# Performance work log

Hardware: AMD Instinct MI355X
Metric: run time of the kernel (lower is better)

Reference implementation:

```python
import jax, jax.numpy as jnp
import numpy as np

N = 100000
E = 1600000
IN_C, HID_C, OUT_C = 128, 256, 40


def sage_conv(x, src, dst, W_l, W_r, b):
    # mean aggregation of source-node features into destination nodes
    msgs = x[src]                                            # [E, d]
    agg = jax.ops.segment_sum(msgs, dst, num_segments=N)     # [N, d]
    deg = jax.ops.segment_sum(jnp.ones((src.shape[0],), x.dtype), dst,
                              num_segments=N)                # [N]
    agg = agg / jnp.clip(deg, 1.0, None)[:, None]
    # out = lin_l(agg) + lin_r(x); weights stored [out, in] like torch
    return agg @ W_l.T + x @ W_r.T + b


def setup_inputs() -> dict:
    key = jax.random.key(0)
    ks = jax.random.split(key, 10)
    s = 0.05
    x = jax.random.normal(ks[0], (N, IN_C), dtype=jnp.float32)
    edge_index = jax.random.randint(ks[1], (2, E), 0, N, dtype=jnp.int64)
    return {
        "x": x,
        "edge_index": edge_index,
        "W_l0": jax.random.normal(ks[2], (HID_C, IN_C), dtype=jnp.float32) * s,
        "W_r0": jax.random.normal(ks[3], (HID_C, IN_C), dtype=jnp.float32) * s,
        "b0": jnp.zeros((HID_C,), jnp.float32),
        "W_l1": jax.random.normal(ks[4], (HID_C, HID_C), dtype=jnp.float32) * s,
        "W_r1": jax.random.normal(ks[5], (HID_C, HID_C), dtype=jnp.float32) * s,
        "b1": jnp.zeros((HID_C,), jnp.float32),
        "W_lo": jax.random.normal(ks[6], (OUT_C, HID_C), dtype=jnp.float32) * s,
        "W_ro": jax.random.normal(ks[7], (OUT_C, HID_C), dtype=jnp.float32) * s,
        "bo": jnp.zeros((OUT_C,), jnp.float32),
    }


def reference(x, edge_index, W_l0, W_r0, b0, W_l1, W_r1, b1, W_lo, W_ro, bo):
    src, dst = edge_index[0], edge_index[1]
    h = jax.nn.relu(sage_conv(x, src, dst, W_l0, W_r0, b0))
    h = jax.nn.relu(sage_conv(h, src, dst, W_l1, W_r1, b1))
    out = sage_conv(h, src, dst, W_lo, W_ro, bo)
    return jax.nn.log_softmax(out, axis=1)
```

## Files before the change

### kernel.cpp

```cpp
#include <hip/hip_runtime.h>
#include <hip/hip_bf16.h>
#include <cstdint>
#include <cstddef>

#define NN   100000
#define NE   1600000
#define HID  256
#define OUTC 40

typedef __attribute__((ext_vector_type(8))) short bf16x8;
typedef __attribute__((ext_vector_type(4))) float f32x4;

static __device__ __forceinline__ ushort f2bf(float f) {
    __hip_bfloat16 h = __float2bfloat16(f);
    return *reinterpret_cast<ushort*>(&h);
}
static __device__ __forceinline__ float bflo(unsigned u) { return __uint_as_float(u << 16); }
static __device__ __forceinline__ float bfhi(unsigned u) { return __uint_as_float(u & 0xffff0000u); }
static __device__ __forceinline__ float sb(unsigned w, int k) {
    return (float)((int)(w << (24 - 8 * k)) >> 24);
}

__global__ void k_count(const int* __restrict__ dst, int* __restrict__ cnt) {
    int i = blockIdx.x * blockDim.x + threadIdx.x;
    if (i < NE) atomicAdd(&cnt[dst[i]], 1);
}

__global__ void k_blocksum(const int* __restrict__ cnt, int* __restrict__ bsum) {
    __shared__ int s[256];
    int t = threadIdx.x;
    int n = blockIdx.x * 256 + t;
    s[t] = (n < NN) ? cnt[n] : 0;
    __syncthreads();
    for (int off = 128; off; off >>= 1) {
        if (t < off) s[t] += s[t + off];
        __syncthreads();
    }
    if (t == 0) bsum[blockIdx.x] = s[0];
}

__global__ void k_scanblock(const int* __restrict__ bsum, int* __restrict__ boff, int nb) {
    __shared__ int s[512];
    int t = threadIdx.x;
    int v = (t < nb) ? bsum[t] : 0;
    s[t] = v;
    __syncthreads();
    for (int off = 1; off < 512; off <<= 1) {
        int u = (t >= off) ? s[t - off] : 0;
        __syncthreads();
        s[t] += u;
        __syncthreads();
    }
    if (t < nb) boff[t] = s[t] - v;
}

__global__ void k_rowptr(const int* __restrict__ cnt, const int* __restrict__ boff,
                         int* __restrict__ rowptr, int* __restrict__ fillp,
                         float* __restrict__ invd) {
    __shared__ int s[256];
    int t = threadIdx.x;
    int n = blockIdx.x * 256 + t;
    int c = (n < NN) ? cnt[n] : 0;
    s[t] = c;
    __syncthreads();
    for (int off = 1; off < 256; off <<= 1) {
        int u = (t >= off) ? s[t - off] : 0;
        __syncthreads();
        s[t] += u;
        __syncthreads();
    }
    if (n < NN) {
        int excl = boff[blockIdx.x] + s[t] - c;
        rowptr[n] = excl;
        fillp[n]  = excl;
        invd[n]   = 1.0f / (float)(c > 1 ? c : 1);
    }
    if (n == 0) rowptr[NN] = NE;
}

__global__ void k_fill(const int* __restrict__ src, const int* __restrict__ dst,
                       int* __restrict__ fillp, int* __restrict__ colidx) {
    int i = blockIdx.x * blockDim.x + threadIdx.x;
    if (i < NE) {
        int p = atomicAdd(&fillp[dst[i]], 1);
        colidx[p] = src[i];
    }
}

__global__ void k_cvtfrag(const float* __restrict__ W, ushort* __restrict__ dst,
                          int ocreal, int d, int nf) {
    int f = blockIdx.x * 256 + threadIdx.x;
    if (f >= nf) return;
    int lm = f & 15, lk = (f >> 4) & 3;
    int rest = f >> 6;
    int dk = d / 32;
    int kk = rest % dk, cc = rest / dk;
    int row = cc * 16 + lm, col = kk * 32 + lk * 8;
    unsigned q0 = 0, q1 = 0, q2 = 0, q3 = 0;
    if (row < ocreal) {
        const float4* p = (const float4*)(W + (size_t)row * d + col);
        float4 a = p[0], b = p[1];
        q0 = (unsigned)f2bf(a.x) | ((unsigned)f2bf(a.y) << 16);
        q1 = (unsigned)f2bf(a.z) | ((unsigned)f2bf(a.w) << 16);
        q2 = (unsigned)f2bf(b.x) | ((unsigned)f2bf(b.y) << 16);
        q3 = (unsigned)f2bf(b.z) | ((unsigned)f2bf(b.w) << 16);
    }
    *(uint4*)(dst + (size_t)f * 8) = make_uint4(q0, q1, q2, q3);
}

__global__ __launch_bounds__(256) void k_quant_x4(const float* __restrict__ x,
                                                  unsigned* __restrict__ xq4,
                                                  float* __restrict__ sx4) {
    int t = threadIdx.x;
    int qw = t >> 4, ql = t & 15;
    int row = blockIdx.x * 16 + qw;
    if (row >= NN) return;
    const float4* p = (const float4*)(x + (size_t)row * 128 + ql * 8);
    float4 a = p[0], b = p[1];
    float v[8] = {a.x, a.y, a.z, a.w, b.x, b.y, b.z, b.w};
    float m = 0.f;
    #pragma unroll
    for (int k = 0; k < 8; ++k) m = fmaxf(m, fabsf(v[k]));
    m = fmaxf(m, __shfl_xor(m, 1));
    m = fmaxf(m, __shfl_xor(m, 2));
    m = fmaxf(m, __shfl_xor(m, 4));
    m = fmaxf(m, __shfl_xor(m, 8));
    float inv = (m > 0.f) ? 7.f / m : 0.f;
    unsigned w = 0;
    #pragma unroll
    for (int k = 0; k < 8; ++k)
        w |= ((unsigned)(int)rintf(v[k] * inv) & 15u) << (4 * k);
    xq4[(size_t)row * 16 + ql] = w;
    if (ql == 0) sx4[row] = (m > 0.f) ? m / 7.f : 0.f;
}

__global__ __launch_bounds__(256) void k_quant_h84(const ushort* __restrict__ h,
                                                   char* __restrict__ hq8, float* __restrict__ s8,
                                                   unsigned* __restrict__ hq4, float* __restrict__ s4) {
    int t = threadIdx.x;
    int qw = t >> 4, ql = t & 15;
    int row = blockIdx.x * 16 + qw;
    if (row >= NN) return;
    const uint4* p = (const uint4*)(h + (size_t)row * 256 + ql * 16);
    uint4 a = p[0], b = p[1];
    float v[16];
    v[0]  = bflo(a.x); v[1]  = bfhi(a.x); v[2]  = bflo(a.y); v[3]  = bfhi(a.y);
    v[4]  = bflo(a.z); v[5]  = bfhi(a.z); v[6]  = bflo(a.w); v[7]  = bfhi(a.w);
    v[8]  = bflo(b.x); v[9]  = bfhi(b.x); v[10] = bflo(b.y); v[11] = bfhi(b.y);
    v[12] = bflo(b.z); v[13] = bfhi(b.z); v[14] = bflo(b.w); v[15] = bfhi(b.w);
    float m = 0.f;
    #pragma unroll
    for (int k = 0; k < 16; ++k) m = fmaxf(m, v[k]);
    m = fmaxf(m, __shfl_xor(m, 1));
    m = fmaxf(m, __shfl_xor(m, 2));
    m = fmaxf(m, __shfl_xor(m, 4));
    m = fmaxf(m, __shfl_xor(m, 8));
    float inv8 = (m > 0.f) ? 127.f / m : 0.f;
    float inv4 = (m > 0.f) ? 15.f / m : 0.f;
    unsigned wo[4];
    #pragma unroll
    for (int wi = 0; wi < 4; ++wi) {
        unsigned w = 0;
        #pragma unroll
        for (int k = 0; k < 4; ++k)
            w |= ((unsigned)(unsigned char)(char)(int)rintf(v[wi * 4 + k] * inv8)) << (8 * k);
        wo[wi] = w;
    }
    *(uint4*)(hq8 + (size_t)row * 256 + ql * 16) = make_uint4(wo[0], wo[1], wo[2], wo[3]);
    unsigned lo = 0, hi = 0;
    #pragma unroll
    for (int k = 0; k < 8; ++k)
        lo |= ((unsigned)(int)rintf(v[k] * inv4) & 15u) << (4 * k);
    #pragma unroll
    for (int k = 0; k < 8; ++k)
        hi |= ((unsigned)(int)rintf(v[8 + k] * inv4) & 15u) << (4 * k);
    *(uint2*)(hq4 + (size_t)row * 32 + ql * 2) = make_uint2(lo, hi);
    if (ql == 0) {
        s8[row] = (m > 0.f) ? m / 127.f : 0.f;
        s4[row] = (m > 0.f) ? m / 15.f  : 0.f;
    }
}

template<int D, bool SELF_F32, bool SIGNED>
__global__ __launch_bounds__(256, 4) void k_layer4(
    const unsigned* __restrict__ qin4, const float* __restrict__ qs4,
    const void* __restrict__ selfp, const float* __restrict__ selfs,
    const ushort* __restrict__ Wl, const ushort* __restrict__ Wr,
    const float* __restrict__ bias, const float* __restrict__ invd,
    const int* __restrict__ rowptr, const int* __restrict__ colidx,
    ushort* __restrict__ hout)
{
    __shared__ ushort aggS[64 * D];
    __shared__ int cidxS[2048];
    char* aggSb = (char*)aggS;
    const int t  = threadIdx.x;
    const int r0 = blockIdx.x * 64;
    constexpr int LPR = D / 16;
    constexpr int GPB = 256 / LPR;
    constexpr int RW  = D / 8;
    const int gid = t / LPR, li = t % LPR;

    const int ebase = rowptr[r0];
    const int rend  = (r0 + 64 < NN) ? (r0 + 64) : NN;
    const int etot  = rowptr[rend] - ebase;
    const bool inlds = (etot <= 2048);
    if (inlds) {
        for (int i = t; i < etot; i += 256) cidxS[i] = colidx[ebase + i];
    }
    __syncthreads();

    for (int rr = gid; rr < 64; rr += GPB) {
        const int r = r0 + rr;
        float acc[16];
        #pragma unroll
        for (int k = 0; k < 16; ++k) acc[k] = 0.f;
        if (r < NN) {
            const int beg = rowptr[r], end = rowptr[r + 1];
            for (int e = beg; e < end; e += 8) {
                int sidx[8];
                if (inlds) {
                    #pragma unroll
                    for (int j = 0; j < 8; ++j)
                        sidx[j] = (e + j < end) ? cidxS[e + j - ebase] : -1;
                } else {
                    #pragma unroll
                    for (int j = 0; j < 8; ++j)
                        sidx[j] = (e + j < end) ? colidx[e + j] : -1;
                }
                uint2 u[8]; float sc[8];
                #pragma unroll
                for (int j = 0; j < 8; ++j) {
                    if (sidx[j] >= 0) {
                        u[j]  = *(const uint2*)(qin4 + (size_t)sidx[j] * RW + li * 2);
                        sc[j] = qs4[sidx[j]];
                    } else { u[j] = make_uint2(0u, 0u); sc[j] = 0.f; }
                }
                #pragma unroll
                for (int j = 0; j < 8; ++j) {
                    #pragma unroll
                    for (int wi = 0; wi < 2; ++wi) {
                        unsigned w = wi ? u[j].y : u[j].x;
                        #pragma unroll
                        for (int k = 0; k < 8; ++k) {
                            float f;
                            if (SIGNED) f = (float)((int)(w << (28 - 4 * k)) >> 28);
                            else        f = (float)((w >> (4 * k)) & 15u);
                            acc[wi * 8 + k] = fmaf(sc[j], f, acc[wi * 8 + k]);
                        }
                    }
                }
            }
            const float iv = invd[r];
            #pragma unroll
            for (int k = 0; k < 16; ++k) acc[k] *= iv;
        }
        #pragma unroll
        for (int gg = 0; gg < 2; ++gg) {
            unsigned q0 = (unsigned)f2bf(acc[gg*8+0]) | ((unsigned)f2bf(acc[gg*8+1]) << 16);
            unsigned q1 = (unsigned)f2bf(acc[gg*8+2]) | ((unsigned)f2bf(acc[gg*8+3]) << 16);
            unsigned q2 = (unsigned)f2bf(acc[gg*8+4]) | ((unsigned)f2bf(acc[gg*8+5]) << 16);
            unsigned q3 = (unsigned)f2bf(acc[gg*8+6]) | ((unsigned)f2bf(acc[gg*8+7]) << 16);
            int g  = li * 2 + gg;
            int gs = g ^ (rr & 7);
            *(uint4*)(aggSb + (size_t)rr * (D * 2) + (gs << 4)) = make_uint4(q0, q1, q2, q3);
        }
    }
    __syncthreads();

    const int w = t >> 6, l = t & 63, lm = l & 15, lk = l >> 4;
    const int rr = w * 16 + lm;
    const int rg = r0 + rr;

    bf16x8 ax[D / 32];
    if (SELF_F32) {
        const float* xf = (const float*)selfp;
        #pragma unroll
        for (int kk = 0; kk < D / 32; ++kk) {
            bf16x8 v;
            if (rg < NN) {
                const float4* p = (const float4*)(xf + (size_t)rg * D + kk * 32 + lk * 8);
                float4 f0 = p[0], f1 = p[1];
                v[0] = (short)f2bf(f0.x); v[1] = (short)f2bf(f0.y);
                v[2] = (short)f2bf(f0.z); v[3] = (short)f2bf(f0.w);
                v[4] = (short)f2bf(f1.x); v[5] = (short)f2bf(f1.y);
                v[6] = (short)f2bf(f1.z); v[7] = (short)f2bf(f1.w);
            } else v = (bf16x8)(short)0;
            ax[kk] = v;
        }
    } else {
        const char* hq = (const char*)selfp;
        const float sr = (rg < NN) ? selfs[rg] : 0.f;
        #pragma unroll
        for (int kk = 0; kk < D / 32; ++kk) {
            uint2 uq = (rg < NN)
                ? *(const uint2*)(hq + (size_t)rg * D + kk * 32 + lk * 8)
                : make_uint2(0u, 0u);
            bf16x8 v;
            v[0] = (short)f2bf(sr * sb(uq.x, 0));
            v[1] = (short)f2bf(sr * sb(uq.x, 1));
            v[2] = (short)f2bf(sr * sb(uq.x, 2));
            v[3] = (short)f2bf(sr * sb(uq.x, 3));
            v[4] = (short)f2bf(sr * sb(uq.y, 0));
            v[5] = (short)f2bf(sr * sb(uq.y, 1));
            v[6] = (short)f2bf(sr * sb(uq.y, 2));
            v[7] = (short)f2bf(sr * sb(uq.y, 3));
            ax[kk] = v;
        }
    }

    for (int cc = 0; cc < HID / 16; ++cc) {
        const int c = cc * 16 + lm;
        f32x4 acc = {0.f, 0.f, 0.f, 0.f};
        #pragma unroll
        for (int kk = 0; kk < D / 32; ++kk) {
            int g  = kk * 4 + lk;
            int gs = g ^ (rr & 7);
            bf16x8 a_agg = *(const bf16x8*)(aggSb + (size_t)rr * (D * 2) + (gs << 4));
            const size_t wf = ((size_t)(cc * (D / 32) + kk) * 64 + l) * 8;
            bf16x8 bl = *(const bf16x8*)(Wl + wf);
            bf16x8 br = *(const bf16x8*)(Wr + wf);
            acc = __builtin_amdgcn_mfma_f32_16x16x32_bf16(a_agg, bl, acc, 0, 0, 0);
            acc = __builtin_amdgcn_mfma_f32_16x16x32_bf16(ax[kk], br, acc, 0, 0, 0);
        }
        const float bv = bias[c];
        #pragma unroll
        for (int i = 0; i < 4; ++i) {
            const int orow = r0 + w * 16 + lk * 4 + i;
            if (orow < NN) {
                float v = fmaxf(acc[i] + bv, 0.f);
                hout[(size_t)orow * HID + c] = f2bf(v);
            }
        }
    }
}

__global__ __launch_bounds__(256, 4) void k_premul(
    const ushort* __restrict__ h1, const ushort* __restrict__ wlo,
    const ushort* __restrict__ wro, const float* __restrict__ bo,
    char* __restrict__ qq, float* __restrict__ sq, float* __restrict__ rbuf)
{
    const int t = threadIdx.x;
    const int r0 = blockIdx.x * 64;
    const int w = t >> 6, l = t & 63, lm = l & 15, lk = l >> 4;
    const int rr = w * 16 + lm;
    const int rg = r0 + rr;

    f32x4 aq[3], ar[3];
    #pragma unroll
    for (int cc = 0; cc < 3; ++cc) { aq[cc] = {0.f,0.f,0.f,0.f}; ar[cc] = {0.f,0.f,0.f,0.f}; }

    #pragma unroll
    for (int kk = 0; kk < 8; ++kk) {
        bf16x8 a = (rg < NN)
            ? *(const bf16x8*)(h1 + (size_t)rg * 256 + kk * 32 + lk * 8)
            : (bf16x8)(short)0;
        #pragma unroll
        for (int cc = 0; cc < 3; ++cc) {
            const size_t wf = ((size_t)(cc * 8 + kk) * 64 + l) * 8;
            bf16x8 bl = *(const bf16x8*)(wlo + wf);
            bf16x8 br = *(const bf16x8*)(wro + wf);
            aq[cc] = __builtin_amdgcn_mfma_f32_16x16x32_bf16(a, bl, aq[cc], 0, 0, 0);
            ar[cc] = __builtin_amdgcn_mfma_f32_16x16x32_bf16(a, br, ar[cc], 0, 0, 0);
        }
    }

    #pragma unroll
    for (int i = 0; i < 4; ++i) {
        const int orow = r0 + w * 16 + lk * 4 + i;
        if (orow >= NN) continue;
        float m = 0.f;
        #pragma unroll
        for (int cc = 0; cc < 3; ++cc) {
            const int c = cc * 16 + lm;
            if (c < OUTC) m = fmaxf(m, fabsf(aq[cc][i]));
        }
        m = fmaxf(m, __shfl_xor(m, 1));
        m = fmaxf(m, __shfl_xor(m, 2));
        m = fmaxf(m, __shfl_xor(m, 4));
        m = fmaxf(m, __shfl_xor(m, 8));
        const float inv = (m > 0.f) ? 127.f / m : 0.f;
        #pragma unroll
        for (int cc = 0; cc < 3; ++cc) {
            const int c = cc * 16 + lm;
            char qv = (c < OUTC) ? (char)(int)rintf(aq[cc][i] * inv) : (char)0;
            qq[(size_t)orow * 64 + c] = qv;
            rbuf[(size_t)orow * 64 + c] = (c < OUTC) ? (ar[cc][i] + bo[c]) : 0.f;
        }
        qq[(size_t)orow * 64 + 48 + lm] = (char)0;
        rbuf[(size_t)orow * 64 + 48 + lm] = 0.f;
        if (lm == 0) sq[orow] = m / 127.f;
    }
}

__global__ __launch_bounds__(256) void k_final(
    const char* __restrict__ qq, const float* __restrict__ sq,
    const float* __restrict__ rbuf, const float* __restrict__ invd,
    const int* __restrict__ rowptr, const int* __restrict__ colidx,
    float* __restrict__ out)
{
    const int t = threadIdx.x;
    const int g = t >> 2, li = t & 3;
    const int row = blockIdx.x * 64 + g;
    if (row >= NN) return;

    float acc[16];
    #pragma unroll
    for (int k = 0; k < 16; ++k) acc[k] = 0.f;

    const int beg = rowptr[row], end = rowptr[row + 1];
    for (int e = beg; e < end; e += 8) {
        int sidx[8];
        #pragma unroll
        for (int j = 0; j < 8; ++j) sidx[j] = (e + j < end) ? colidx[e + j] : -1;
        uint4 u[8]; float sc[8];
        #pragma unroll
        for (int j = 0; j < 8; ++j) {
            if (sidx[j] >= 0) {
                u[j]  = *(const uint4*)(qq + (size_t)sidx[j] * 64 + li * 16);
                sc[j] = sq[sidx[j]];
            } else { u[j] = make_uint4(0u, 0u, 0u, 0u); sc[j] = 0.f; }
        }
        #pragma unroll
        for (int j = 0; j < 8; ++j) {
            #pragma unroll
            for (int wi = 0; wi < 4; ++wi) {
                unsigned w = (&u[j].x)[wi];
                acc[wi*4+0] = fmaf(sc[j], sb(w, 0), acc[wi*4+0]);
                acc[wi*4+1] = fmaf(sc[j], sb(w, 1), acc[wi*4+1]);
                acc[wi*4+2] = fmaf(sc[j], sb(w, 2), acc[wi*4+2]);
                acc[wi*4+3] = fmaf(sc[j], sb(w, 3), acc[wi*4+3]);
            }
        }
    }

    const float iv = invd[row];
    const float4* rp = (const float4*)(rbuf + (size_t)row * 64 + li * 16);
    float v[16];
    #pragma unroll
    for (int ch = 0; ch < 4; ++ch) {
        float4 rv = rp[ch];
        v[ch*4+0] = acc[ch*4+0] * iv + rv.x;
        v[ch*4+1] = acc[ch*4+1] * iv + rv.y;
        v[ch*4+2] = acc[ch*4+2] * iv + rv.z;
        v[ch*4+3] = acc[ch*4+3] * iv + rv.w;
    }
    #pragma unroll
    for (int k = 0; k < 16; ++k)
        if (li * 16 + k >= OUTC) v[k] = -INFINITY;

    float m = v[0];
    #pragma unroll
    for (int k = 1; k < 16; ++k) m = fmaxf(m, v[k]);
    m = fmaxf(m, __shfl_xor(m, 1));
    m = fmaxf(m, __shfl_xor(m, 2));

    float s = 0.f;
    #pragma unroll
    for (int k = 0; k < 16; ++k)
        if (li * 16 + k < OUTC) s += __expf(v[k] - m);
    s += __shfl_xor(s, 1);
    s += __shfl_xor(s, 2);
    const float ls = __logf(s);

    #pragma unroll
    for (int ch = 0; ch < 4; ++ch) {
        const int c = li * 16 + ch * 4;
        if (c < OUTC) {
            float4 o;
            o.x = v[ch*4+0] - m - ls;
            o.y = v[ch*4+1] - m - ls;
            o.z = v[ch*4+2] - m - ls;
            o.w = v[ch*4+3] - m - ls;
            *(float4*)(out + (size_t)row * OUTC + c) = o;
        }
    }
}

extern "C" void kernel_launch(void* const* d_in, const int* in_sizes, int n_in,
                              void* d_out, int out_size, void* d_ws, size_t ws_size,
                              hipStream_t stream) {
    const float* x   = (const float*)d_in[0];
    const int*   ei  = (const int*)d_in[1];
    const int*   src = ei;
    const int*   dst = ei + NE;
    const float* Wl0 = (const float*)d_in[2];
    const float* Wr0 = (const float*)d_in[3];
    const float* b0  = (const float*)d_in[4];
    const float* Wl1 = (const float*)d_in[5];
    const float* Wr1 = (const float*)d_in[6];
    const float* b1  = (const float*)d_in[7];
    const float* Wlo = (const float*)d_in[8];
    const float* Wro = (const float*)d_in[9];
    const float* bo  = (const float*)d_in[10];
    float* out = (float*)d_out;

    char* ws = (char*)d_ws;
    const size_t MB = 1 << 20;
    float*    invd   = (float*)(ws + 0);
    int*      rowptr = (int*)(ws + MB / 2);
    int*      cnt    = (int*)(ws + MB);
    int*      fillp  = (int*)(ws + MB + MB / 2);
    int*      bsum   = (int*)(ws + 2 * MB);
    int*      boff   = (int*)(ws + 2 * MB + MB / 4);
    float*    sx4    = (float*)(ws + 2 * MB + MB / 2);
    float*    s8     = (float*)(ws + 3 * MB);
    float*    s4     = (float*)(ws + 3 * MB + MB / 2);
    float*    sq     = (float*)(ws + 4 * MB);
    ushort*   Wb     = (ushort*)(ws + 4 * MB + MB / 2);
    int*      colidx = (int*)(ws + 5 * MB + MB / 2);
    unsigned* xq4    = (unsigned*)(ws + 12 * MB);
    char*     qq     = (char*)(ws + 12 * MB);
    unsigned* h0q4   = (unsigned*)(ws + 19 * MB);
    ushort*   h0     = (ushort*)(ws + 32 * MB);
    ushort*   h1     = (ushort*)(ws + 32 * MB);
    char*     h0q8   = (char*)(ws + 84 * MB);
    float*    rbuf   = (float*)(ws + 84 * MB);

    ushort* wl0 = Wb;
    ushort* wr0 = Wb + 32768;
    ushort* wl1 = Wb + 65536;
    ushort* wr1 = Wb + 131072;
    ushort* wlo = Wb + 196608;
    ushort* wro = Wb + 208896;

    hipMemsetAsync(cnt, 0, NN * sizeof(int), stream);
    k_count<<<(NE + 255) / 256, 256, 0, stream>>>(dst, cnt);
    const int NB = (NN + 255) / 256;
    k_blocksum<<<NB, 256, 0, stream>>>(cnt, bsum);
    k_scanblock<<<1, 512, 0, stream>>>(bsum, boff, NB);
    k_rowptr<<<NB, 256, 0, stream>>>(cnt, boff, rowptr, fillp, invd);
    k_fill<<<(NE + 255) / 256, 256, 0, stream>>>(src, dst, fillp, colidx);

    k_cvtfrag<<<16, 256, 0, stream>>>(Wl0, wl0, 256, 128, 4096);
    k_cvtfrag<<<16, 256, 0, stream>>>(Wr0, wr0, 256, 128, 4096);
    k_cvtfrag<<<32, 256, 0, stream>>>(Wl1, wl1, 256, 256, 8192);
    k_cvtfrag<<<32, 256, 0, stream>>>(Wr1, wr1, 256, 256, 8192);
    k_cvtfrag<<<6,  256, 0, stream>>>(Wlo, wlo, 40, 256, 1536);
    k_cvtfrag<<<6,  256, 0, stream>>>(Wro, wro, 40, 256, 1536);
    k_quant_x4<<<(NN + 15) / 16, 256, 0, stream>>>(x, xq4, sx4);

    const int GB = (NN + 63) / 64;
    k_layer4<128, true, true><<<GB, 256, 0, stream>>>(
        xq4, sx4, x, nullptr, wl0, wr0, b0, invd, rowptr, colidx, h0);
    k_quant_h84<<<(NN + 15) / 16, 256, 0, stream>>>(h0, h0q8, s8, h0q4, s4);
    k_layer4<256, false, false><<<GB, 256, 0, stream>>>(
        h0q4, s4, h0q8, s8, wl1, wr1, b1, invd, rowptr, colidx, h1);
    k_premul<<<GB, 256, 0, stream>>>(h1, wlo, wro, bo, qq, sq, rbuf);
    k_final<<<(NN + 63) / 64, 256, 0, stream>>>(qq, sq, rbuf, invd, rowptr, colidx, out);
}
```

Measured before the change: 522.8 us.

## Switch gathers from int4 to unsigned int8 with shuffle-broadcast neighbor indices

Replaces the 4-bit quantized neighbor features with 8-bit unsigned (offset-128 for signed inputs, with a sum-of-scales correction) for both SAGE layers and the final layer. Neighbor indices and scales are now loaded once per lane and broadcast via warp shuffles instead of each lane reloading them. k_final also stages column indices in LDS. The layer-2 self path reuses the same 8-bit buffer, so the separate int4 copy is no longer written. The gather traffic per edge doubles (8 bytes to 16 bytes per lane) in exchange for higher precision and cheaper index loads.

```diff
diff --git a/kernel.cpp b/kernel.cpp
--- a/kernel.cpp
+++ b/kernel.cpp
@@ -17,8 +17,8 @@
 }
 static __device__ __forceinline__ float bflo(unsigned u) { return __uint_as_float(u << 16); }
 static __device__ __forceinline__ float bfhi(unsigned u) { return __uint_as_float(u & 0xffff0000u); }
-static __device__ __forceinline__ float sb(unsigned w, int k) {
-    return (float)((int)(w << (24 - 8 * k)) >> 24);
+static __device__ __forceinline__ float ubf(unsigned w, int k) {
+    return (float)((w >> (8 * k)) & 255u);
 }
 
 __global__ void k_count(const int* __restrict__ dst, int* __restrict__ cnt) {
@@ -108,9 +108,9 @@
     *(uint4*)(dst + (size_t)f * 8) = make_uint4(q0, q1, q2, q3);
 }
 
-__global__ __launch_bounds__(256) void k_quant_x4(const float* __restrict__ x,
-                                                  unsigned* __restrict__ xq4,
-                                                  float* __restrict__ sx4) {
+__global__ __launch_bounds__(256) void k_quant_x8(const float* __restrict__ x,
+                                                  unsigned char* __restrict__ xq,
+                                                  float* __restrict__ sx) {
     int t = threadIdx.x;
     int qw = t >> 4, ql = t & 15;
     int row = blockIdx.x * 16 + qw;
@@ -125,18 +125,21 @@
     m = fmaxf(m, __shfl_xor(m, 2));
     m = fmaxf(m, __shfl_xor(m, 4));
     m = fmaxf(m, __shfl_xor(m, 8));
-    float inv = (m > 0.f) ? 7.f / m : 0.f;
-    unsigned w = 0;
-    #pragma unroll
-    for (int k = 0; k < 8; ++k)
-        w |= ((unsigned)(int)rintf(v[k] * inv) & 15u) << (4 * k);
-    xq4[(size_t)row * 16 + ql] = w;
-    if (ql == 0) sx4[row] = (m > 0.f) ? m / 7.f : 0.f;
-}
-
-__global__ __launch_bounds__(256) void k_quant_h84(const ushort* __restrict__ h,
-                                                   char* __restrict__ hq8, float* __restrict__ s8,
-                                                   unsigned* __restrict__ hq4, float* __restrict__ s4) {
+    float inv = (m > 0.f) ? 127.f / m : 0.f;
+    unsigned w0 = 0, w1 = 0;
+    #pragma unroll
+    for (int k = 0; k < 4; ++k)
+        w0 |= ((unsigned)((int)rintf(v[k] * inv) + 128) & 255u) << (8 * k);
+    #pragma unroll
+    for (int k = 0; k < 4; ++k)
+        w1 |= ((unsigned)((int)rintf(v[4 + k] * inv) + 128) & 255u) << (8 * k);
+    *(uint2*)(xq + (size_t)row * 128 + ql * 8) = make_uint2(w0, w1);
+    if (ql == 0) sx[row] = (m > 0.f) ? m / 127.f : 0.f;
+}
+
+__global__ __launch_bounds__(256) void k_quant_h8(const ushort* __restrict__ h,
+                                                  unsigned char* __restrict__ hq,
+                                                  float* __restrict__ s8) {
     int t = threadIdx.x;
     int qw = t >> 4, ql = t & 15;
     int row = blockIdx.x * 16 + qw;
@@ -155,36 +158,24 @@
     m = fmaxf(m, __shfl_xor(m, 2));
     m = fmaxf(m, __shfl_xor(m, 4));
     m = fmaxf(m, __shfl_xor(m, 8));
-    float inv8 = (m > 0.f) ? 127.f / m : 0.f;
-    float inv4 = (m > 0.f) ? 15.f / m : 0.f;
+    float inv = (m > 0.f) ? 255.f / m : 0.f;
     unsigned wo[4];
     #pragma unroll
     for (int wi = 0; wi < 4; ++wi) {
         unsigned w = 0;
         #pragma unroll
         for (int k = 0; k < 4; ++k)
-            w |= ((unsigned)(unsigned char)(char)(int)rintf(v[wi * 4 + k] * inv8)) << (8 * k);
+            w |= ((unsigned)(int)rintf(v[wi * 4 + k] * inv) & 255u) << (8 * k);
         wo[wi] = w;
     }
-    *(uint4*)(hq8 + (size_t)row * 256 + ql * 16) = make_uint4(wo[0], wo[1], wo[2], wo[3]);
-    unsigned lo = 0, hi = 0;
-    #pragma unroll
-    for (int k = 0; k < 8; ++k)
-        lo |= ((unsigned)(int)rintf(v[k] * inv4) & 15u) << (4 * k);
-    #pragma unroll
-    for (int k = 0; k < 8; ++k)
-        hi |= ((unsigned)(int)rintf(v[8 + k] * inv4) & 15u) << (4 * k);
-    *(uint2*)(hq4 + (size_t)row * 32 + ql * 2) = make_uint2(lo, hi);
-    if (ql == 0) {
-        s8[row] = (m > 0.f) ? m / 127.f : 0.f;
-        s4[row] = (m > 0.f) ? m / 15.f  : 0.f;
-    }
-}
-
-template<int D, bool SELF_F32, bool SIGNED>
-__global__ __launch_bounds__(256, 4) void k_layer4(
-    const unsigned* __restrict__ qin4, const float* __restrict__ qs4,
-    const void* __restrict__ selfp, const float* __restrict__ selfs,
+    *(uint4*)(hq + (size_t)row * 256 + ql * 16) = make_uint4(wo[0], wo[1], wo[2], wo[3]);
+    if (ql == 0) s8[row] = (m > 0.f) ? m / 255.f : 0.f;
+}
+
+template<int D, bool SELF_F32, bool BIASED>
+__global__ __launch_bounds__(256, 4) void k_layer8u(
+    const unsigned char* __restrict__ qin, const float* __restrict__ qs,
+    const float* __restrict__ xf,
     const ushort* __restrict__ Wl, const ushort* __restrict__ Wr,
     const float* __restrict__ bias, const float* __restrict__ invd,
     const int* __restrict__ rowptr, const int* __restrict__ colidx,
@@ -197,8 +188,10 @@
     const int r0 = blockIdx.x * 64;
     constexpr int LPR = D / 16;
     constexpr int GPB = 256 / LPR;
-    constexpr int RW  = D / 8;
+    constexpr int RSH = (D == 128) ? 7 : 8;
     const int gid = t / LPR, li = t % LPR;
+    const int l = t & 63;
+    const int base = l & ~(LPR - 1);
 
     const int ebase = rowptr[r0];
     const int rend  = (r0 + 64 < NN) ? (r0 + 64) : NN;
@@ -214,45 +207,46 @@
         float acc[16];
         #pragma unroll
         for (int k = 0; k < 16; ++k) acc[k] = 0.f;
+        float sum_sc = 0.f;
         if (r < NN) {
             const int beg = rowptr[r], end = rowptr[r + 1];
             for (int e = beg; e < end; e += 8) {
-                int sidx[8];
-                if (inlds) {
-                    #pragma unroll
-                    for (int j = 0; j < 8; ++j)
-                        sidx[j] = (e + j < end) ? cidxS[e + j - ebase] : -1;
-                } else {
-                    #pragma unroll
-                    for (int j = 0; j < 8; ++j)
-                        sidx[j] = (e + j < end) ? colidx[e + j] : -1;
-                }
-                uint2 u[8]; float sc[8];
+                const int myi = e + (li & 7);
+                int se = -1;
+                if (myi < end) se = inlds ? cidxS[myi - ebase] : colidx[myi];
+                float mysc = (se >= 0) ? qs[se] : 0.f;
+                int   sj[8];
+                float sc[8];
+                uint4 u[8];
+                #pragma unroll
+                for (int j = 0; j < 8; ++j) sj[j] = __shfl(se, base + j);
+                #pragma unroll
+                for (int j = 0; j < 8; ++j) sc[j] = __shfl(mysc, base + j);
                 #pragma unroll
                 for (int j = 0; j < 8; ++j) {
-                    if (sidx[j] >= 0) {
-                        u[j]  = *(const uint2*)(qin4 + (size_t)sidx[j] * RW + li * 2);
-                        sc[j] = qs4[sidx[j]];
-                    } else { u[j] = make_uint2(0u, 0u); sc[j] = 0.f; }
+                    u[j] = (sj[j] >= 0)
+                        ? *(const uint4*)(qin + (((unsigned)sj[j]) << RSH) + (li << 4))
+                        : make_uint4(0u, 0u, 0u, 0u);
                 }
                 #pragma unroll
                 for (int j = 0; j < 8; ++j) {
                     #pragma unroll
-                    for (int wi = 0; wi < 2; ++wi) {
-                        unsigned w = wi ? u[j].y : u[j].x;
-                        #pragma unroll
-                        for (int k = 0; k < 8; ++k) {
-                            float f;
-                            if (SIGNED) f = (float)((int)(w << (28 - 4 * k)) >> 28);
-                            else        f = (float)((w >> (4 * k)) & 15u);
-                            acc[wi * 8 + k] = fmaf(sc[j], f, acc[wi * 8 + k]);
-                        }
+                    for (int wi = 0; wi < 4; ++wi) {
+                        unsigned w = (&u[j].x)[wi];
+                        acc[wi*4+0] = fmaf(sc[j], ubf(w, 0), acc[wi*4+0]);
+                        acc[wi*4+1] = fmaf(sc[j], ubf(w, 1), acc[wi*4+1]);
+                        acc[wi*4+2] = fmaf(sc[j], ubf(w, 2), acc[wi*4+2]);
+                        acc[wi*4+3] = fmaf(sc[j], ubf(w, 3), acc[wi*4+3]);
                     }
+                    if (BIASED) sum_sc += sc[j];
                 }
             }
             const float iv = invd[r];
             #pragma unroll
-            for (int k = 0; k < 16; ++k) acc[k] *= iv;
+            for (int k = 0; k < 16; ++k) {
+                if (BIASED) acc[k] = (acc[k] - 128.f * sum_sc) * iv;
+                else        acc[k] = acc[k] * iv;
+            }
         }
         #pragma unroll
         for (int gg = 0; gg < 2; ++gg) {
@@ -267,13 +261,12 @@
     }
     __syncthreads();
 
-    const int w = t >> 6, l = t & 63, lm = l & 15, lk = l >> 4;
+    const int w = t >> 6, lm = l & 15, lk = l >> 4;
     const int rr = w * 16 + lm;
     const int rg = r0 + rr;
 
     bf16x8 ax[D / 32];
     if (SELF_F32) {
-        const float* xf = (const float*)selfp;
         #pragma unroll
         for (int kk = 0; kk < D / 32; ++kk) {
             bf16x8 v;
@@ -288,22 +281,21 @@
             ax[kk] = v;
         }
     } else {
-        const char* hq = (const char*)selfp;
-        const float sr = (rg < NN) ? selfs[rg] : 0.f;
+        const float sr = (rg < NN) ? qs[rg] : 0.f;
         #pragma unroll
         for (int kk = 0; kk < D / 32; ++kk) {
             uint2 uq = (rg < NN)
-                ? *(const uint2*)(hq + (size_t)rg * D + kk * 32 + lk * 8)
+                ? *(const uint2*)(qin + (((unsigned)rg) << RSH) + kk * 32 + lk * 8)
                 : make_uint2(0u, 0u);
             bf16x8 v;
-            v[0] = (short)f2bf(sr * sb(uq.x, 0));
-            v[1] = (short)f2bf(sr * sb(uq.x, 1));
-            v[2] = (short)f2bf(sr * sb(uq.x, 2));
-            v[3] = (short)f2bf(sr * sb(uq.x, 3));
-            v[4] = (short)f2bf(sr * sb(uq.y, 0));
-            v[5] = (short)f2bf(sr * sb(uq.y, 1));
-            v[6] = (short)f2bf(sr * sb(uq.y, 2));
-            v[7] = (short)f2bf(sr * sb(uq.y, 3));
+            v[0] = (short)f2bf(sr * ubf(uq.x, 0));
+            v[1] = (short)f2bf(sr * ubf(uq.x, 1));
+            v[2] = (short)f2bf(sr * ubf(uq.x, 2));
+            v[3] = (short)f2bf(sr * ubf(uq.x, 3));
+            v[4] = (short)f2bf(sr * ubf(uq.y, 0));
+            v[5] = (short)f2bf(sr * ubf(uq.y, 1));
+            v[6] = (short)f2bf(sr * ubf(uq.y, 2));
+            v[7] = (short)f2bf(sr * ubf(uq.y, 3));
             ax[kk] = v;
         }
     }
@@ -337,7 +329,7 @@
 __global__ __launch_bounds__(256, 4) void k_premul(
     const ushort* __restrict__ h1, const ushort* __restrict__ wlo,
     const ushort* __restrict__ wro, const float* __restrict__ bo,
-    char* __restrict__ qq, float* __restrict__ sq, float* __restrict__ rbuf)
+    unsigned char* __restrict__ qq, float* __restrict__ sq, float* __restrict__ rbuf)
 {
     const int t = threadIdx.x;
     const int r0 = blockIdx.x * 64;
@@ -382,54 +374,77 @@
         #pragma unroll
         for (int cc = 0; cc < 3; ++cc) {
             const int c = cc * 16 + lm;
-            char qv = (c < OUTC) ? (char)(int)rintf(aq[cc][i] * inv) : (char)0;
-            qq[(size_t)orow * 64 + c] = qv;
+            int code = (c < OUTC) ? (int)rintf(aq[cc][i] * inv) : 0;
+            qq[(size_t)orow * 64 + c] = (unsigned char)(code + 128);
             rbuf[(size_t)orow * 64 + c] = (c < OUTC) ? (ar[cc][i] + bo[c]) : 0.f;
         }
-        qq[(size_t)orow * 64 + 48 + lm] = (char)0;
+        qq[(size_t)orow * 64 + 48 + lm] = (unsigned char)128;
         rbuf[(size_t)orow * 64 + 48 + lm] = 0.f;
         if (lm == 0) sq[orow] = m / 127.f;
     }
 }
 
 __global__ __launch_bounds__(256) void k_final(
-    const char* __restrict__ qq, const float* __restrict__ sq,
+    const unsigned char* __restrict__ qq, const float* __restrict__ sq,
     const float* __restrict__ rbuf, const float* __restrict__ invd,
     const int* __restrict__ rowptr, const int* __restrict__ colidx,
     float* __restrict__ out)
 {
+    __shared__ int cidxS[2048];
     const int t = threadIdx.x;
     const int g = t >> 2, li = t & 3;
-    const int row = blockIdx.x * 64 + g;
+    const int r0 = blockIdx.x * 64;
+    const int row = r0 + g;
+    const int l = t & 63;
+    const int base = l & ~3;
+
+    const int ebase = rowptr[r0];
+    const int rend  = (r0 + 64 < NN) ? (r0 + 64) : NN;
+    const int etot  = rowptr[rend] - ebase;
+    const bool inlds = (etot <= 2048);
+    if (inlds) {
+        for (int i = t; i < etot; i += 256) cidxS[i] = colidx[ebase + i];
+    }
+    __syncthreads();
     if (row >= NN) return;
 
     float acc[16];
     #pragma unroll
     for (int k = 0; k < 16; ++k) acc[k] = 0.f;
+    float sum_sc = 0.f;
 
     const int beg = rowptr[row], end = rowptr[row + 1];
     for (int e = beg; e < end; e += 8) {
-        int sidx[8];
-        #pragma unroll
-        for (int j = 0; j < 8; ++j) sidx[j] = (e + j < end) ? colidx[e + j] : -1;
-        uint4 u[8]; float sc[8];
+        const int m0 = e + li, m1 = e + 4 + li;
+        int se0 = -1, se1 = -1;
+        if (m0 < end) se0 = inlds ? cidxS[m0 - ebase] : colidx[m0];
+        if (m1 < end) se1 = inlds ? cidxS[m1 - ebase] : colidx[m1];
+        float ms0 = (se0 >= 0) ? sq[se0] : 0.f;
+        float ms1 = (se1 >= 0) ? sq[se1] : 0.f;
+        int   sj[8];
+        float sc[8];
+        uint4 u[8];
+        #pragma unroll
+        for (int j = 0; j < 4; ++j) { sj[j] = __shfl(se0, base + j); sc[j] = __shfl(ms0, base + j); }
+        #pragma unroll
+        for (int j = 4; j < 8; ++j) { sj[j] = __shfl(se1, base + j - 4); sc[j] = __shfl(ms1, base + j - 4); }
         #pragma unroll
         for (int j = 0; j < 8; ++j) {
-            if (sidx[j] >= 0) {
-                u[j]  = *(const uint4*)(qq + (size_t)sidx[j] * 64 + li * 16);
-                sc[j] = sq[sidx[j]];
-            } else { u[j] = make_uint4(0u, 0u, 0u, 0u); sc[j] = 0.f; }
+            u[j] = (sj[j] >= 0)
+                ? *(const uint4*)(qq + (((unsigned)sj[j]) << 6) + (li << 4))
+                : make_uint4(0u, 0u, 0u, 0u);
         }
         #pragma unroll
         for (int j = 0; j < 8; ++j) {
             #pragma unroll
             for (int wi = 0; wi < 4; ++wi) {
                 unsigned w = (&u[j].x)[wi];
-                acc[wi*4+0] = fmaf(sc[j], sb(w, 0), acc[wi*4+0]);
-                acc[wi*4+1] = fmaf(sc[j], sb(w, 1), acc[wi*4+1]);
-                acc[wi*4+2] = fmaf(sc[j], sb(w, 2), acc[wi*4+2]);
-                acc[wi*4+3] = fmaf(sc[j], sb(w, 3), acc[wi*4+3]);
+                acc[wi*4+0] = fmaf(sc[j], ubf(w, 0), acc[wi*4+0]);
+                acc[wi*4+1] = fmaf(sc[j], ubf(w, 1), acc[wi*4+1]);
+                acc[wi*4+2] = fmaf(sc[j], ubf(w, 2), acc[wi*4+2]);
+                acc[wi*4+3] = fmaf(sc[j], ubf(w, 3), acc[wi*4+3]);
             }
+            sum_sc += sc[j];
         }
     }
 
@@ -439,10 +454,10 @@
     #pragma unroll
     for (int ch = 0; ch < 4; ++ch) {
         float4 rv = rp[ch];
-        v[ch*4+0] = acc[ch*4+0] * iv + rv.x;
-        v[ch*4+1] = acc[ch*4+1] * iv + rv.y;
-        v[ch*4+2] = acc[ch*4+2] * iv + rv.z;
-        v[ch*4+3] = acc[ch*4+3] * iv + rv.w;
+        v[ch*4+0] = (acc[ch*4+0] - 128.f * sum_sc) * iv + rv.x;
+        v[ch*4+1] = (acc[ch*4+1] - 128.f * sum_sc) * iv + rv.y;
+        v[ch*4+2] = (acc[ch*4+2] - 128.f * sum_sc) * iv + rv.z;
+        v[ch*4+3] = (acc[ch*4+3] - 128.f * sum_sc) * iv + rv.w;
     }
     #pragma unroll
     for (int k = 0; k < 16; ++k)
@@ -496,25 +511,23 @@
 
     char* ws = (char*)d_ws;
     const size_t MB = 1 << 20;
-    float*    invd   = (float*)(ws + 0);
-    int*      rowptr = (int*)(ws + MB / 2);
-    int*      cnt    = (int*)(ws + MB);
-    int*      fillp  = (int*)(ws + MB + MB / 2);
-    int*      bsum   = (int*)(ws + 2 * MB);
-    int*      boff   = (int*)(ws + 2 * MB + MB / 4);
-    float*    sx4    = (float*)(ws + 2 * MB + MB / 2);
-    float*    s8     = (float*)(ws + 3 * MB);
-    float*    s4     = (float*)(ws + 3 * MB + MB / 2);
-    float*    sq     = (float*)(ws + 4 * MB);
-    ushort*   Wb     = (ushort*)(ws + 4 * MB + MB / 2);
-    int*      colidx = (int*)(ws + 5 * MB + MB / 2);
-    unsigned* xq4    = (unsigned*)(ws + 12 * MB);
-    char*     qq     = (char*)(ws + 12 * MB);
-    unsigned* h0q4   = (unsigned*)(ws + 19 * MB);
-    ushort*   h0     = (ushort*)(ws + 32 * MB);
-    ushort*   h1     = (ushort*)(ws + 32 * MB);
-    char*     h0q8   = (char*)(ws + 84 * MB);
-    float*    rbuf   = (float*)(ws + 84 * MB);
+    float*         invd   = (float*)(ws + 0);
+    int*           rowptr = (int*)(ws + MB / 2);
+    int*           cnt    = (int*)(ws + MB);
+    int*           fillp  = (int*)(ws + MB + MB / 2);
+    int*           bsum   = (int*)(ws + 2 * MB);
+    int*           boff   = (int*)(ws + 2 * MB + MB / 4);
+    float*         sx     = (float*)(ws + 2 * MB + MB / 2);
+    float*         s8     = (float*)(ws + 3 * MB);
+    float*         sq     = (float*)(ws + 4 * MB);
+    ushort*        Wb     = (ushort*)(ws + 4 * MB + MB / 2);
+    int*           colidx = (int*)(ws + 5 * MB + MB / 2);
+    unsigned char* xq8    = (unsigned char*)(ws + 12 * MB);
+    unsigned char* qq     = (unsigned char*)(ws + 12 * MB);
+    ushort*        h0     = (ushort*)(ws + 32 * MB);
+    ushort*        h1     = (ushort*)(ws + 32 * MB);
+    unsigned char* h0q8u  = (unsigned char*)(ws + 84 * MB);
+    float*         rbuf   = (float*)(ws + 84 * MB);
 
     ushort* wl0 = Wb;
     ushort* wr0 = Wb + 32768;
@@ -537,14 +550,14 @@
     k_cvtfrag<<<32, 256, 0, stream>>>(Wr1, wr1, 256, 256, 8192);
     k_cvtfrag<<<6,  256, 0, stream>>>(Wlo, wlo, 40, 256, 1536);
     k_cvtfrag<<<6,  256, 0, stream>>>(Wro, wro, 40, 256, 1536);
-    k_quant_x4<<<(NN + 15) / 16, 256, 0, stream>>>(x, xq4, sx4);
+    k_quant_x8<<<(NN + 15) / 16, 256, 0, stream>>>(x, xq8, sx);
 
     const int GB = (NN + 63) / 64;
-    k_layer4<128, true, true><<<GB, 256, 0, stream>>>(
-        xq4, sx4, x, nullptr, wl0, wr0, b0, invd, rowptr, colidx, h0);
-    k_quant_h84<<<(NN + 15) / 16, 256, 0, stream>>>(h0, h0q8, s8, h0q4, s4);
-    k_layer4<256, false, false><<<GB, 256, 0, stream>>>(
-        h0q4, s4, h0q8, s8, wl1, wr1, b1, invd, rowptr, colidx, h1);
+    k_layer8u<128, true, true><<<GB, 256, 0, stream>>>(
+        xq8, sx, x, wl0, wr0, b0, invd, rowptr, colidx, h0);
+    k_quant_h8<<<(NN + 15) / 16, 256, 0, stream>>>(h0, h0q8u, s8);
+    k_layer8u<256, false, false><<<GB, 256, 0, stream>>>(
+        h0q8u, s8, nullptr, wl1, wr1, b1, invd, rowptr, colidx, h1);
     k_premul<<<GB, 256, 0, stream>>>(h1, wlo, wro, bo, qq, sq, rbuf);
     k_final<<<(NN + 63) / 64, 256, 0, stream>>>(qq, sq, rbuf, invd, rowptr, colidx, out);
 }
```

New measurement: 513.4 us. Within noise of the previous version (-1.8%).
